# Kernel tuning notes

Hardware: AMD Instinct MI355X
Metric: run time of the kernel (lower is better)

The kernel has to match this reference:

```python
import jax, jax.numpy as jnp
import numpy as np

N_NODES = 50000
N_EDGES = 800000
IN_CH = 128
HID = 64
OUT_CH = 64


def sage_conv(x, src, dst, w_l, w_r, b, num_nodes):
    """PyG SAGEConv with mean aggregation: lin_l(mean_j x_j) + lin_r(x_i)."""
    # gather source features and scatter-mean into destination nodes
    agg = jax.ops.segment_sum(x[src], dst, num_segments=num_nodes)          # [N, C]
    deg = jax.ops.segment_sum(jnp.ones((src.shape[0],), x.dtype), dst,
                              num_segments=num_nodes)                        # [N]
    mean = agg / jnp.maximum(deg, 1.0)[:, None]
    return mean @ w_l + x @ w_r + b


def setup_inputs() -> dict:
    key = jax.random.key(0)
    k = jax.random.split(key, 8)
    x = jax.random.normal(k[0], (N_NODES, IN_CH), dtype=jnp.float32)
    edge_index = jax.random.randint(k[1], (2, N_EDGES), 0, N_NODES, dtype=jnp.int32)
    s1 = 1.0 / np.sqrt(IN_CH)
    s2 = 1.0 / np.sqrt(HID)
    w1_l = jax.random.uniform(k[2], (IN_CH, HID), jnp.float32, -s1, s1)
    w1_r = jax.random.uniform(k[3], (IN_CH, HID), jnp.float32, -s1, s1)
    b1 = jax.random.uniform(k[4], (HID,), jnp.float32, -s1, s1)
    w2_l = jax.random.uniform(k[5], (HID, OUT_CH), jnp.float32, -s2, s2)
    w2_r = jax.random.uniform(k[6], (HID, OUT_CH), jnp.float32, -s2, s2)
    b2 = jax.random.uniform(k[7], (OUT_CH,), jnp.float32, -s2, s2)
    return {"x": x, "edge_index": edge_index,
            "w1_l": w1_l, "w1_r": w1_r, "b1": b1,
            "w2_l": w2_l, "w2_r": w2_r, "b2": b2}


def reference(x, edge_index, w1_l, w1_r, b1, w2_l, w2_r, b2):
    src, dst = edge_index[0], edge_index[1]
    num_nodes = x.shape[0]
    h = jax.nn.relu(sage_conv(x, src, dst, w1_l, w1_r, b1, num_nodes))
    out = jax.nn.relu(sage_conv(h, src, dst, w2_l, w2_r, b2, num_nodes))
    return out
```

## Files before the change

kernel.cpp:

```cpp
#include <hip/hip_runtime.h>
#include <hip/hip_fp16.h>

#define DEGCAP 64
#define NBKT 391
#define BCAP 2560
#define TILE 4000
#define SUBB 4

typedef _Float16 half8 __attribute__((ext_vector_type(8)));
typedef float float4v __attribute__((ext_vector_type(4)));

template <int NS>
__device__ __forceinline__ void load_bfrag(const float* __restrict__ Wl,
                                           const float* __restrict__ Wr,
                                           int col, int qd,
                                           half8* bl, half8* br) {
    #pragma unroll
    for (int s = 0; s < NS; ++s) {
        half8 hl, hr;
        #pragma unroll
        for (int i = 0; i < 8; ++i) {
            int k = s * 32 + qd * 8 + i;
            hl[i] = (_Float16)Wl[k * 64 + col];
            hr[i] = (_Float16)Wr[k * 64 + col];
        }
        bl[s] = hl;
        br[s] = hr;
    }
}

template <int K, int MT>
__device__ __forceinline__ void gemm_body_f32(const float* __restrict__ Av,
                                              const float* __restrict__ Wl,
                                              const float* __restrict__ Wr,
                                              unsigned short* __restrict__ Clh,
                                              unsigned short* __restrict__ Trh,
                                              int M, int blk) {
    constexpr int NS = K / 32;
    const int tid = threadIdx.x;
    const int row0 = blk * (MT * 16);
    const int wv = tid >> 6;
    const int lane = tid & 63;
    const int qd = lane >> 4;
    const int lr = lane & 15;
    const int col = wv * 16 + lr;

    half8 bl[NS], br[NS];
    load_bfrag<NS>(Wl, Wr, col, qd, bl, br);

    half8 a[MT][NS];
    #pragma unroll
    for (int i = 0; i < MT; ++i) {
        const int gr = row0 + i * 16 + lr;
        const bool ok = gr < M;
        const float* Arow = Av + (long long)gr * K;
        #pragma unroll
        for (int s = 0; s < NS; ++s) {
            float4 t0 = make_float4(0.f, 0.f, 0.f, 0.f);
            float4 t1 = make_float4(0.f, 0.f, 0.f, 0.f);
            if (ok) {
                t0 = *(const float4*)&Arow[s * 32 + qd * 8];
                t1 = *(const float4*)&Arow[s * 32 + qd * 8 + 4];
            }
            half8 h;
            h[0] = (_Float16)t0.x; h[1] = (_Float16)t0.y;
            h[2] = (_Float16)t0.z; h[3] = (_Float16)t0.w;
            h[4] = (_Float16)t1.x; h[5] = (_Float16)t1.y;
            h[6] = (_Float16)t1.z; h[7] = (_Float16)t1.w;
            a[i][s] = h;
        }
    }

    float4v accL[MT], accR[MT];
    #pragma unroll
    for (int i = 0; i < MT; ++i) {
        accL[i] = (float4v){0.f, 0.f, 0.f, 0.f};
        accR[i] = (float4v){0.f, 0.f, 0.f, 0.f};
    }

    #pragma unroll
    for (int i = 0; i < MT; ++i) {
        #pragma unroll
        for (int s = 0; s < NS; ++s) {
            accL[i] = __builtin_amdgcn_mfma_f32_16x16x32_f16(a[i][s], bl[s], accL[i], 0, 0, 0);
            accR[i] = __builtin_amdgcn_mfma_f32_16x16x32_f16(a[i][s], br[s], accR[i], 0, 0, 0);
        }
    }

    #pragma unroll
    for (int i = 0; i < MT; ++i) {
        #pragma unroll
        for (int rg = 0; rg < 4; ++rg) {
            int gr = row0 + i * 16 + qd * 4 + rg;
            if (gr < M) {
                Clh[(long long)gr * 64 + col] = __half_as_ushort(__float2half_rn(accL[i][rg]));
                Trh[(long long)gr * 64 + col] = __half_as_ushort(__float2half_rn(accR[i][rg]));
            }
        }
    }
}

__global__ __launch_bounds__(256) void fused_scatter_gemm1(
        const int* __restrict__ src, const int* __restrict__ dst,
        int* __restrict__ bCursor, unsigned int* __restrict__ gPacked,
        int E, int scatterBlocks,
        const float* __restrict__ A,
        const float* __restrict__ w1l, const float* __restrict__ w1r,
        unsigned short* __restrict__ Clh, unsigned short* __restrict__ Trh,
        int M) {
    __shared__ __align__(16) char smem[19200];
    const int tid = threadIdx.x;

    if ((int)blockIdx.x < scatterBlocks) {
        unsigned int* spv = (unsigned int*)smem;
        int* hist = (int*)(smem + 16000);
        int* cur  = (int*)(smem + 17600);

        const int t0 = blockIdx.x * TILE;
        const int len = (E - t0) < TILE ? (E - t0) : TILE;

        for (int i = tid; i < 400; i += 256) hist[i] = 0;
        __syncthreads();
        for (int j = tid; j < len; j += 256) {
            unsigned int d = (unsigned int)dst[t0 + j];
            unsigned int s = (unsigned int)src[t0 + j];
            spv[j] = (d << 16) | s;
            atomicAdd(&hist[d >> 7], 1);
        }
        __syncthreads();
        for (int t = tid; t < NBKT; t += 256)
            if (hist[t] > 0)
                cur[t] = t * BCAP + atomicAdd(&bCursor[t], hist[t]);
        __syncthreads();
        for (int j = tid; j < len; j += 256) {
            unsigned int v = spv[j];
            int b = (int)(v >> 23);
            int pos = atomicAdd(&cur[b], 1);
            if (pos < (b + 1) * BCAP) gPacked[pos] = v;
        }
    } else {
        gemm_body_f32<128, 2>(A, w1l, w1r, Clh, Trh, M,
                              (int)blockIdx.x - scatterBlocks);
    }
}

__global__ __launch_bounds__(256) void bb_agg1_gemm2(
        const unsigned int* __restrict__ gPacked,
        const int* __restrict__ bCursor,
        const uint2* __restrict__ TL, const uint2* __restrict__ TR,
        const float* __restrict__ bias,
        const float* __restrict__ w2l, const float* __restrict__ w2r,
        unsigned short* __restrict__ ssrc_out,
        int* __restrict__ deg_out,
        unsigned short* __restrict__ Cl2,
        unsigned short* __restrict__ Tr2,
        int N) {
    __shared__ unsigned short ssrcT[32 * 64];
    __shared__ int cnt[32];
    __shared__ int degL[32];
    __shared__ _Float16 xs[32 * 72];
    const int tid = threadIdx.x;
    const int B = (int)blockIdx.x >> 2;
    const int oct = (int)blockIdx.x & 3;
    const int node0 = B * 128 + oct * 32;
    const int grp = node0 >> 5;

    if (tid < 32) cnt[tid] = 0;
    __syncthreads();
    int C = bCursor[B];
    if (C > BCAP) C = BCAP;
    const unsigned int* gp = gPacked + B * BCAP;
    for (int j = tid; j < C; j += 256) {
        unsigned int v = gp[j];
        if ((int)(v >> 21) == grp) {
            int l = (int)(v >> 16) & 31;
            int pos = atomicAdd(&cnt[l], 1);
            if (pos < DEGCAP)
                ssrcT[l * 64 + pos] = (unsigned short)(v & 0xFFFFu);
        }
    }
    __syncthreads();
    if (tid < 32) {
        int d = cnt[tid] < DEGCAP ? cnt[tid] : DEGCAP;
        degL[tid] = d;
        int node = node0 + tid;
        if (node < N) deg_out[node] = d;
    }
    __syncthreads();
    {
        const uint2* s2 = (const uint2*)ssrcT;
        for (int i = tid; i < 32 * 16; i += 256) {
            int node = node0 + (i >> 4);
            if (node < N)
                ((uint2*)ssrc_out)[(size_t)node * 16 + (i & 15)] = s2[i];
        }
    }

    const int wv = tid >> 6;
    const int lane = tid & 63;
    const int c = lane & 15;
    const int g = lane >> 4;
    for (int r = 0; r < 2; ++r) {
        const int l = r * 16 + wv * 4 + g;
        const int w = node0 + l;
        const bool ok = w < N;
        const int n = ok ? degL[l] : 0;
        const unsigned short* row = &ssrcT[l * 64];
        float a0 = 0.f, a1 = 0.f, a2 = 0.f, a3 = 0.f;
        for (int j = 0; j < n; j += 4) {
            uint2 ids = *(const uint2*)&row[j];
            int e0 = (int)(ids.x & 0xFFFFu);
            int e1 = (int)(ids.x >> 16);
            int e2 = (int)(ids.y & 0xFFFFu);
            int e3 = (int)(ids.y >> 16);
            uint2 q0 = TL[e0 * 16 + c];
            uint2 q1 = TL[e1 * 16 + c];
            uint2 q2 = TL[e2 * 16 + c];
            uint2 q3 = TL[e3 * 16 + c];
            float2 f;
            f = __half22float2(*(__half2*)&q0.x); a0 += f.x; a1 += f.y;
            f = __half22float2(*(__half2*)&q0.y); a2 += f.x; a3 += f.y;
            if (j + 1 < n) {
                f = __half22float2(*(__half2*)&q1.x); a0 += f.x; a1 += f.y;
                f = __half22float2(*(__half2*)&q1.y); a2 += f.x; a3 += f.y;
            }
            if (j + 2 < n) {
                f = __half22float2(*(__half2*)&q2.x); a0 += f.x; a1 += f.y;
                f = __half22float2(*(__half2*)&q2.y); a2 += f.x; a3 += f.y;
            }
            if (j + 3 < n) {
                f = __half22float2(*(__half2*)&q3.x); a0 += f.x; a1 += f.y;
                f = __half22float2(*(__half2*)&q3.y); a2 += f.x; a3 += f.y;
            }
        }
        float4 h = make_float4(0.f, 0.f, 0.f, 0.f);
        if (ok) {
            float d = (float)(n > 1 ? n : 1);
            uint2 tu = TR[(size_t)w * 16 + c];
            float2 t0 = __half22float2(*(__half2*)&tu.x);
            float2 t1 = __half22float2(*(__half2*)&tu.y);
            float4 bb = *(const float4*)&bias[c * 4];
            h.x = fmaxf(a0 / d + t0.x + bb.x, 0.f);
            h.y = fmaxf(a1 / d + t0.y + bb.y, 0.f);
            h.z = fmaxf(a2 / d + t1.x + bb.z, 0.f);
            h.w = fmaxf(a3 / d + t1.y + bb.w, 0.f);
        }
        __half2 h0 = __floats2half2_rn(h.x, h.y);
        __half2 h1 = __floats2half2_rn(h.z, h.w);
        uint2 st;
        st.x = *(unsigned int*)&h0;
        st.y = *(unsigned int*)&h1;
        *(uint2*)&xs[l * 72 + c * 4] = st;
    }
    __syncthreads();

    const int qd = lane >> 4;
    const int lr = lane & 15;
    const int col = wv * 16 + lr;

    half8 bl[2], br[2], a[2][2];
    load_bfrag<2>(w2l, w2r, col, qd, bl, br);
    #pragma unroll
    for (int s = 0; s < 2; ++s)
        #pragma unroll
        for (int i = 0; i < 2; ++i)
            a[i][s] = *(const half8*)&xs[(i * 16 + lr) * 72 + s * 32 + qd * 8];

    float4v accL[2], accR[2];
    #pragma unroll
    for (int i = 0; i < 2; ++i) {
        accL[i] = (float4v){0.f, 0.f, 0.f, 0.f};
        accR[i] = (float4v){0.f, 0.f, 0.f, 0.f};
    }
    #pragma unroll
    for (int i = 0; i < 2; ++i) {
        #pragma unroll
        for (int s = 0; s < 2; ++s) {
            accL[i] = __builtin_amdgcn_mfma_f32_16x16x32_f16(a[i][s], bl[s], accL[i], 0, 0, 0);
            accR[i] = __builtin_amdgcn_mfma_f32_16x16x32_f16(a[i][s], br[s], accR[i], 0, 0, 0);
        }
    }

    #pragma unroll
    for (int i = 0; i < 2; ++i) {
        #pragma unroll
        for (int rg = 0; rg < 4; ++rg) {
            int gr = node0 + i * 16 + qd * 4 + rg;
            if (gr < N) {
                Cl2[(long long)gr * 64 + col] = __half_as_ushort(__float2half_rn(accL[i][rg]));
                Tr2[(long long)gr * 64 + col] = __half_as_ushort(__float2half_rn(accR[i][rg]));
            }
        }
    }
}

__global__ __launch_bounds__(256) void agg2(const uint2* __restrict__ TL,
                                            const uint2* __restrict__ TR,
                                            const float* __restrict__ bias,
                                            const int* __restrict__ deg_,
                                            const uint2* __restrict__ ssrc2,
                                            float* __restrict__ outv, int N) {
    __shared__ unsigned short ssrcT[16 * 64];
    __shared__ int degL[16];
    const int tid = threadIdx.x;
    const int node0 = (int)blockIdx.x * 16;

    {
        int node = node0 + (tid >> 4);
        uint2 v = (node < N) ? ssrc2[(size_t)node * 16 + (tid & 15)]
                             : make_uint2(0u, 0u);
        *(uint2*)&ssrcT[(tid >> 4) * 64 + (tid & 15) * 4] = v;
    }
    if (tid < 16) {
        int node = node0 + tid;
        degL[tid] = (node < N) ? deg_[node] : 0;
    }
    __syncthreads();

    const int wv = tid >> 6;
    const int lane = tid & 63;
    const int c = lane & 15;
    const int l = wv * 4 + (lane >> 4);
    const int w = node0 + l;
    const bool ok = w < N;
    const int n = ok ? degL[l] : 0;
    const unsigned short* row = &ssrcT[l * 64];

    float a0 = 0.f, a1 = 0.f, a2 = 0.f, a3 = 0.f;
    for (int j = 0; j < n; j += 8) {
        uint2 i0 = *(const uint2*)&row[j];
        uint2 i1 = *(const uint2*)&row[j + 4];
        int e0 = (int)(i0.x & 0xFFFFu);
        int e1 = (int)(i0.x >> 16);
        int e2 = (int)(i0.y & 0xFFFFu);
        int e3 = (int)(i0.y >> 16);
        int e4 = (int)(i1.x & 0xFFFFu);
        int e5 = (int)(i1.x >> 16);
        int e6 = (int)(i1.y & 0xFFFFu);
        int e7 = (int)(i1.y >> 16);
        uint2 q0 = TL[e0 * 16 + c];
        uint2 q1 = TL[e1 * 16 + c];
        uint2 q2 = TL[e2 * 16 + c];
        uint2 q3 = TL[e3 * 16 + c];
        uint2 q4 = TL[e4 * 16 + c];
        uint2 q5 = TL[e5 * 16 + c];
        uint2 q6 = TL[e6 * 16 + c];
        uint2 q7 = TL[e7 * 16 + c];
        float2 f;
        f = __half22float2(*(__half2*)&q0.x); a0 += f.x; a1 += f.y;
        f = __half22float2(*(__half2*)&q0.y); a2 += f.x; a3 += f.y;
        if (j + 1 < n) {
            f = __half22float2(*(__half2*)&q1.x); a0 += f.x; a1 += f.y;
            f = __half22float2(*(__half2*)&q1.y); a2 += f.x; a3 += f.y;
        }
        if (j + 2 < n) {
            f = __half22float2(*(__half2*)&q2.x); a0 += f.x; a1 += f.y;
            f = __half22float2(*(__half2*)&q2.y); a2 += f.x; a3 += f.y;
        }
        if (j + 3 < n) {
            f = __half22float2(*(__half2*)&q3.x); a0 += f.x; a1 += f.y;
            f = __half22float2(*(__half2*)&q3.y); a2 += f.x; a3 += f.y;
        }
        if (j + 4 < n) {
            f = __half22float2(*(__half2*)&q4.x); a0 += f.x; a1 += f.y;
            f = __half22float2(*(__half2*)&q4.y); a2 += f.x; a3 += f.y;
        }
        if (j + 5 < n) {
            f = __half22float2(*(__half2*)&q5.x); a0 += f.x; a1 += f.y;
            f = __half22float2(*(__half2*)&q5.y); a2 += f.x; a3 += f.y;
        }
        if (j + 6 < n) {
            f = __half22float2(*(__half2*)&q6.x); a0 += f.x; a1 += f.y;
            f = __half22float2(*(__half2*)&q6.y); a2 += f.x; a3 += f.y;
        }
        if (j + 7 < n) {
            f = __half22float2(*(__half2*)&q7.x); a0 += f.x; a1 += f.y;
            f = __half22float2(*(__half2*)&q7.y); a2 += f.x; a3 += f.y;
        }
    }

    if (ok) {
        float d = (float)(n > 1 ? n : 1);
        uint2 tu = TR[(size_t)w * 16 + c];
        float2 t0 = __half22float2(*(__half2*)&tu.x);
        float2 t1 = __half22float2(*(__half2*)&tu.y);
        float4 bb = *(const float4*)&bias[c * 4];
        float v0 = fmaxf(a0 / d + t0.x + bb.x, 0.f);
        float v1 = fmaxf(a1 / d + t0.y + bb.y, 0.f);
        float v2 = fmaxf(a2 / d + t1.x + bb.z, 0.f);
        float v3 = fmaxf(a3 / d + t1.y + bb.w, 0.f);
        ((float4*)outv)[(size_t)w * 16 + c] = make_float4(v0, v1, v2, v3);
    }
}

extern "C" void kernel_launch(void* const* d_in, const int* in_sizes, int n_in,
                              void* d_out, int out_size, void* d_ws, size_t ws_size,
                              hipStream_t stream) {
    const float* x   = (const float*)d_in[0];
    const int*   ei  = (const int*)d_in[1];
    const float* w1l = (const float*)d_in[2];
    const float* w1r = (const float*)d_in[3];
    const float* b1  = (const float*)d_in[4];
    const float* w2l = (const float*)d_in[5];
    const float* w2r = (const float*)d_in[6];
    const float* b2  = (const float*)d_in[7];
    float* out = (float*)d_out;

    const int N = in_sizes[0] / 128;
    const int E = in_sizes[1] / 2;
    const int* src = ei;
    const int* dst = ei + E;

    auto alignup = [](size_t v) { return (v + 255) & ~(size_t)255; };
    char* p = (char*)d_ws;
    int* bCursor = (int*)p;                    p += alignup(400 * sizeof(int));
    int* deg     = (int*)p;                    p += alignup((size_t)N * sizeof(int));
    unsigned int* gPacked = (unsigned int*)p;  p += alignup((size_t)400 * BCAP * sizeof(unsigned int));
    unsigned short* ssrc = (unsigned short*)p; p += alignup((size_t)N * DEGCAP * sizeof(unsigned short));
    const long long NC = (long long)N * 64;
    unsigned short* tlh = (unsigned short*)p;  p += alignup((size_t)NC * sizeof(unsigned short));
    unsigned short* tl2 = (unsigned short*)p;  p += alignup((size_t)NC * sizeof(unsigned short));
    unsigned short* trh = (unsigned short*)p;  p += alignup((size_t)NC * sizeof(unsigned short));
    unsigned short* tr2 = (unsigned short*)p;  p += alignup((size_t)NC * sizeof(unsigned short));

    const int scatterBlocks = (E + TILE - 1) / TILE;
    const int gemmBlocks = (N + 31) / 32;
    const int aggBlocks = (N + 15) / 16;
    const int bbaBlocks = NBKT * SUBB;

    hipMemsetAsync(bCursor, 0, 400 * sizeof(int), stream);

    fused_scatter_gemm1<<<scatterBlocks + gemmBlocks, 256, 0, stream>>>(
        src, dst, bCursor, gPacked, E, scatterBlocks,
        x, w1l, w1r, tlh, trh, N);

    bb_agg1_gemm2<<<bbaBlocks, 256, 0, stream>>>(
        gPacked, bCursor, (const uint2*)tlh, (const uint2*)trh,
        b1, w2l, w2r, ssrc, deg, tl2, tr2, N);

    agg2<<<aggBlocks, 256, 0, stream>>>((const uint2*)tl2,
                                        (const uint2*)tr2,
                                        b2, deg, (const uint2*)ssrc,
                                        out, N);
}
```

Baseline: 149.6 us.

## Bucket edges by 32-node groups so aggregation blocks skip filtering

```diff
diff --git a/kernel.cpp b/kernel.cpp
--- a/kernel.cpp
+++ b/kernel.cpp
@@ -2,10 +2,10 @@
 #include <hip/hip_fp16.h>
 
 #define DEGCAP 64
-#define NBKT 391
-#define BCAP 2560
+#define NBKT 1563
+#define NBKT_PAD 1600
+#define BCAP 768
 #define TILE 4000
-#define SUBB 4
 
 typedef _Float16 half8 __attribute__((ext_vector_type(8)));
 typedef float float4v __attribute__((ext_vector_type(4)));
@@ -108,35 +108,29 @@
         const float* __restrict__ w1l, const float* __restrict__ w1r,
         unsigned short* __restrict__ Clh, unsigned short* __restrict__ Trh,
         int M) {
-    __shared__ __align__(16) char smem[19200];
+    __shared__ __align__(16) int hist[NBKT_PAD];
+    __shared__ __align__(16) int cur[NBKT_PAD];
     const int tid = threadIdx.x;
 
     if ((int)blockIdx.x < scatterBlocks) {
-        unsigned int* spv = (unsigned int*)smem;
-        int* hist = (int*)(smem + 16000);
-        int* cur  = (int*)(smem + 17600);
-
         const int t0 = blockIdx.x * TILE;
         const int len = (E - t0) < TILE ? (E - t0) : TILE;
 
-        for (int i = tid; i < 400; i += 256) hist[i] = 0;
+        for (int i = tid; i < NBKT_PAD; i += 256) hist[i] = 0;
         __syncthreads();
-        for (int j = tid; j < len; j += 256) {
-            unsigned int d = (unsigned int)dst[t0 + j];
-            unsigned int s = (unsigned int)src[t0 + j];
-            spv[j] = (d << 16) | s;
-            atomicAdd(&hist[d >> 7], 1);
-        }
+        for (int j = tid; j < len; j += 256)
+            atomicAdd(&hist[((unsigned int)dst[t0 + j]) >> 5], 1);
         __syncthreads();
         for (int t = tid; t < NBKT; t += 256)
             if (hist[t] > 0)
                 cur[t] = t * BCAP + atomicAdd(&bCursor[t], hist[t]);
         __syncthreads();
         for (int j = tid; j < len; j += 256) {
-            unsigned int v = spv[j];
-            int b = (int)(v >> 23);
+            unsigned int d = (unsigned int)dst[t0 + j];
+            unsigned int s = (unsigned int)src[t0 + j];
+            int b = (int)(d >> 5);
             int pos = atomicAdd(&cur[b], 1);
-            if (pos < (b + 1) * BCAP) gPacked[pos] = v;
+            if (pos < (b + 1) * BCAP) gPacked[pos] = (d << 16) | s;
         }
     } else {
         gemm_body_f32<128, 2>(A, w1l, w1r, Clh, Trh, M,
@@ -160,10 +154,8 @@
     __shared__ int degL[32];
     __shared__ _Float16 xs[32 * 72];
     const int tid = threadIdx.x;
-    const int B = (int)blockIdx.x >> 2;
-    const int oct = (int)blockIdx.x & 3;
-    const int node0 = B * 128 + oct * 32;
-    const int grp = node0 >> 5;
+    const int B = (int)blockIdx.x;
+    const int node0 = B * 32;
 
     if (tid < 32) cnt[tid] = 0;
     __syncthreads();
@@ -172,12 +164,10 @@
     const unsigned int* gp = gPacked + B * BCAP;
     for (int j = tid; j < C; j += 256) {
         unsigned int v = gp[j];
-        if ((int)(v >> 21) == grp) {
-            int l = (int)(v >> 16) & 31;
-            int pos = atomicAdd(&cnt[l], 1);
-            if (pos < DEGCAP)
-                ssrcT[l * 64 + pos] = (unsigned short)(v & 0xFFFFu);
-        }
+        int l = (int)(v >> 16) & 31;
+        int pos = atomicAdd(&cnt[l], 1);
+        if (pos < DEGCAP)
+            ssrcT[l * 64 + pos] = (unsigned short)(v & 0xFFFFu);
     }
     __syncthreads();
     if (tid < 32) {
@@ -413,9 +403,9 @@
 
     auto alignup = [](size_t v) { return (v + 255) & ~(size_t)255; };
     char* p = (char*)d_ws;
-    int* bCursor = (int*)p;                    p += alignup(400 * sizeof(int));
+    int* bCursor = (int*)p;                    p += alignup(NBKT_PAD * sizeof(int));
     int* deg     = (int*)p;                    p += alignup((size_t)N * sizeof(int));
-    unsigned int* gPacked = (unsigned int*)p;  p += alignup((size_t)400 * BCAP * sizeof(unsigned int));
+    unsigned int* gPacked = (unsigned int*)p;  p += alignup((size_t)NBKT_PAD * BCAP * sizeof(unsigned int));
     unsigned short* ssrc = (unsigned short*)p; p += alignup((size_t)N * DEGCAP * sizeof(unsigned short));
     const long long NC = (long long)N * 64;
     unsigned short* tlh = (unsigned short*)p;  p += alignup((size_t)NC * sizeof(unsigned short));
@@ -426,9 +416,9 @@
     const int scatterBlocks = (E + TILE - 1) / TILE;
     const int gemmBlocks = (N + 31) / 32;
     const int aggBlocks = (N + 15) / 16;
-    const int bbaBlocks = NBKT * SUBB;
-
-    hipMemsetAsync(bCursor, 0, 400 * sizeof(int), stream);
+    const int bbaBlocks = NBKT;
+
+    hipMemsetAsync(bCursor, 0, NBKT_PAD * sizeof(int), stream);
 
     fused_scatter_gemm1<<<scatterBlocks + gemmBlocks, 256, 0, stream>>>(
         src, dst, bCursor, gPacked, E, scatterBlocks,
```

New measurement: 156.7 us. 4.7% more time.
